# Performance work log

Hardware: AMD Instinct MI355X
Metric: run time of the kernel (lower is better)

## Reference

```python
import jax, jax.numpy as jnp
import numpy as np

NEG_INF = -1e30

def _rotary_tables(n_pos, d_k):
    # angular_freq = (1/10000)**linspace(0,1,d_k//4), padded with d_k//4 zeros -> d_k//2 freqs
    freqs = (1.0 / 10000.0) ** jnp.linspace(0.0, 1.0, d_k // 4, dtype=jnp.float32)
    freqs = jnp.concatenate([freqs, jnp.zeros(d_k // 4, dtype=jnp.float32)])  # [d_k//2]
    t = jnp.arange(n_pos, dtype=jnp.float32)
    theta = t[:, None] * freqs[None, :]  # [n_pos, d_k//2]
    return jnp.cos(theta), jnp.sin(theta)

def _apply_rotary(x_bhtd, cos, sin):
    # Faithful to torch source: cos/sin are indexed/broadcast along dim -3,
    # which for [B,H,T,D] input is the HEAD axis (original code's quirk).
    c = cos[None, :, None, :]  # [1,H,1,D/2]
    s = sin[None, :, None, :]
    x1, x2 = jnp.split(x_bhtd, 2, axis=-1)
    y1 = x1 * c + x2 * s
    y2 = -x1 * s + x2 * c
    return jnp.concatenate([y1, y2], axis=-1)

def setup_inputs() -> dict:
    key = jax.random.key(0)
    k1, k2, k3 = jax.random.split(key, 3)
    B, S, D = 4, 2048, 2048
    x = jax.random.normal(k1, (B, S, D), dtype=jnp.float32)
    Wqkv = jax.random.normal(k2, (D, 3 * D), dtype=jnp.float32) * (D ** -0.5)
    Wo = jax.random.normal(k3, (D, D), dtype=jnp.float32) * (D ** -0.5)
    return {"x": x, "Wqkv": Wqkv, "Wo": Wo, "n_heads": 16}

def reference(x, Wqkv, Wo, n_heads):
    B, S, D = x.shape
    H = int(n_heads)
    d_k = D // H
    qkv = (x @ Wqkv).reshape(B, S, 3, H, d_k)
    qkv = jnp.transpose(qkv, (2, 0, 3, 1, 4))  # [3,B,H,S,dk]
    Q, K, V = qkv[0], qkv[1], qkv[2]
    cos, sin = _rotary_tables(H, d_k)  # indexed by head axis, per original code
    Q = _apply_rotary(Q, cos, sin)
    K = _apply_rotary(K, cos, sin)
    scores = jnp.einsum('bhqd,bhkd->bhqk', Q, K) / jnp.sqrt(jnp.float32(d_k))
    causal = jnp.tril(jnp.ones((S, S), dtype=bool))
    scores = jnp.where(causal[None, None, :, :], scores, NEG_INF)
    attn = jax.nn.softmax(scores, axis=-1)
    out = jnp.einsum('bhqk,bhkd->bhqd', attn, V)  # [B,H,S,dk]
    out = jnp.transpose(out, (0, 2, 1, 3)).reshape(B, S, D)
    return out @ Wo
```

## Files before the change

kernel.cpp:

```cpp
#include <hip/hip_runtime.h>

typedef __attribute__((ext_vector_type(8))) short short8;
typedef __attribute__((ext_vector_type(4))) short short4v;
typedef __attribute__((ext_vector_type(4))) float f32x4;

__device__ inline short f2bf(float f) {
    union { float f; unsigned u; } v; v.f = f;
    unsigned r = v.u + 0x7fffu + ((v.u >> 16) & 1u);
    return (short)(r >> 16);
}

__device__ __forceinline__ void gload16(const short* g, short* l) {
    __builtin_amdgcn_global_load_lds(
        (const __attribute__((address_space(1))) unsigned int*)g,
        (__attribute__((address_space(3))) unsigned int*)l, 16, 0, 0);
}

__global__ __launch_bounds__(256) void cvt_f32_to_bf16(const float* __restrict__ in,
                                                       short* __restrict__ out, int n4) {
    int i = blockIdx.x * 256 + threadIdx.x;
    if (i >= n4) return;
    float4 v = ((const float4*)in)[i];
    short4v o;
    o[0] = f2bf(v.x); o[1] = f2bf(v.y); o[2] = f2bf(v.z); o[3] = f2bf(v.w);
    ((short4v*)out)[i] = o;
}

__global__ __launch_bounds__(256) void transpose_to_bf16(const float* __restrict__ in,
                                                         short* __restrict__ out,
                                                         int R, int C) {
    __shared__ short tile[64][66];
    int r0 = blockIdx.x * 64, c0 = blockIdx.y * 64;
    int tid = threadIdx.x;
#pragma unroll
    for (int i = 0; i < 16; i++) {
        int idx = i * 256 + tid;
        int r = idx >> 6, c = idx & 63;
        tile[r][c] = f2bf(in[(size_t)(r0 + r) * C + (c0 + c)]);
    }
    __syncthreads();
#pragma unroll
    for (int i = 0; i < 16; i++) {
        int idx = i * 256 + tid;
        int c = idx >> 6, r = idx & 63;
        out[(size_t)(c0 + c) * R + (r0 + r)] = tile[r][c];
    }
}

template <int EPI>
__global__ __launch_bounds__(512) void gemm256(const short* __restrict__ A,
                                               const short* __restrict__ Bt,
                                               int M, int N, int K,
                                               short* __restrict__ O0, short* __restrict__ O1,
                                               short* __restrict__ O2, float* __restrict__ OF,
                                               float qscale) {
    __shared__ short As[2][2][256 * 32];
    __shared__ short Bs[2][2][256 * 32];
    int tid = threadIdx.x, lane = tid & 63, wid = tid >> 6;
    int wr = wid >> 2, wc = wid & 3;
    int mtn = M >> 8;
    int band = mtn >> 3;
    int bid = blockIdx.x;
    int xcd = bid & 7, kk = bid >> 3;
    int nt = kk / band, gmr = kk % band;
    int mt = xcd * band + gmr;
    int row0 = mt << 8, col0 = nt << 8;
    int t15 = lane & 15, t4 = lane >> 4;
    int NT = K >> 6;

    f32x4 acc[8][4];
#pragma unroll
    for (int m = 0; m < 8; m++)
#pragma unroll
        for (int n = 0; n < 4; n++) acc[m][n] = (f32x4){0.f, 0.f, 0.f, 0.f};

    int sg = (lane & 3) ^ ((lane >> 3) & 3);
    int srw = lane >> 2;
    int ce = t4 ^ ((t15 >> 1) & 3);

    auto stageA = [&](int t, int kh) {
        if (t >= NT) return;
        int kb = (t << 6) + (kh << 5);
        short* dst = &As[t & 1][kh][0];
#pragma unroll
        for (int i = 0; i < 2; i++) {
            int seg = wid * 2 + i;
            int row = seg * 16 + srw;
            gload16(A + (size_t)(row0 + row) * K + kb + sg * 8, dst + seg * 512);
        }
    };
    auto stageB = [&](int t, int kh) {
        if (t >= NT) return;
        int kb = (t << 6) + (kh << 5);
        short* dst = &Bs[t & 1][kh][0];
#pragma unroll
        for (int i = 0; i < 2; i++) {
            int seg = wid * 2 + i;
            int row = seg * 16 + srw;
            gload16(Bt + (size_t)(col0 + row) * K + kb + sg * 8, dst + seg * 512);
        }
    };

    auto lda = [&](int d, int kh, short8 (&af)[8]) {
#pragma unroll
        for (int m = 0; m < 8; m++) {
            int row = wr * 128 + m * 16 + t15;
            af[m] = *(short8*)(&As[d][kh][row * 32 + ce * 8]);
        }
    };
    auto ldb = [&](int d, int kh, short8 (&bf)[4]) {
#pragma unroll
        for (int n = 0; n < 4; n++) {
            int row = wc * 64 + n * 16 + t15;
            bf[n] = *(short8*)(&Bs[d][kh][row * 32 + ce * 8]);
        }
    };

#define MFMA32(AF, BF)                                                               \
    __builtin_amdgcn_s_setprio(1);                                                   \
    _Pragma("unroll")                                                                \
    for (int m_ = 0; m_ < 8; m_++)                                                   \
        _Pragma("unroll")                                                            \
        for (int n_ = 0; n_ < 4; n_++)                                               \
            acc[m_][n_] = __builtin_amdgcn_mfma_f32_16x16x32_bf16(                   \
                AF[m_], BF[n_], acc[m_][n_], 0, 0, 0);                               \
    __builtin_amdgcn_s_setprio(0);

    stageA(0, 0); stageB(0, 0);
    stageA(0, 1); stageB(0, 1);
    asm volatile("s_waitcnt vmcnt(0)" ::: "memory");
    asm volatile("s_barrier" ::: "memory");

    for (int t = 0; t < NT; t++) {
        int d = t & 1;
        short8 af0[8], bf0[4], af1[8], bf1[4];
        lda(d, 0, af0); ldb(d, 0, bf0);
        stageA(t + 1, 0); stageB(t + 1, 0);
        stageA(t + 1, 1); stageB(t + 1, 1);
        MFMA32(af0, bf0);
        lda(d, 1, af1); ldb(d, 1, bf1);
        MFMA32(af1, bf1);
        asm volatile("s_waitcnt vmcnt(0)" ::: "memory");
        asm volatile("s_barrier" ::: "memory");
    }

#undef MFMA32

#pragma unroll
    for (int m = 0; m < 8; m++) {
#pragma unroll
        for (int n = 0; n < 4; n++) {
#pragma unroll
            for (int r = 0; r < 4; r++) {
                float v = acc[m][n][r];
                int gm2 = row0 + wr * 128 + m * 16 + t4 * 4 + r;
                int gn = col0 + wc * 64 + n * 16 + t15;
                if (EPI == 0) {
                    int part = gn >> 11, within = gn & 2047;
                    int h = within >> 7, dk = within & 127;
                    int bb = gm2 >> 11, s = gm2 & 2047;
                    int z = bb * 16 + h;
                    if (part == 0) O0[((size_t)z * 2048 + s) * 128 + dk] = f2bf(v * qscale);
                    else if (part == 1) O1[((size_t)z * 2048 + s) * 128 + dk] = f2bf(v);
                    else O2[((size_t)z * 128 + dk) * 2048 + s] = f2bf(v);
                } else {
                    OF[(size_t)gm2 * N + gn] = v;
                }
            }
        }
    }
}

__global__ __launch_bounds__(512, 4) void attn_fwd(const short* __restrict__ Q,
                                                   const short* __restrict__ Kb,
                                                   const short* __restrict__ Vt,
                                                   short* __restrict__ O) {
    __shared__ short Kls[2][64 * 128];
    __shared__ short Vls[128 * 64];
    __shared__ __align__(16) short Pls[8][16 * 64];
    int tid = threadIdx.x, lane = tid & 63, wid = tid >> 6;
    int bx = blockIdx.x, z = blockIdx.y;
    int pr = bx >> 1, hh = bx & 1;
    int qpan = (wid < 4) ? pr : (15 - pr);
    int t15 = lane & 15, t4 = lane >> 4;
    const short* Qh = Q + (size_t)z * 2048 * 128;
    const short* Kh = Kb + (size_t)z * 2048 * 128;
    const short* Vh = Vt + (size_t)z * 128 * 2048;
    int q0w = qpan * 128 + hh * 64 + (wid & 3) * 16;

    short8 qf[4];
    {
        const short* qrow = Qh + (size_t)(q0w + t15) * 128;
#pragma unroll
        for (int s = 0; s < 4; s++) qf[s] = *(const short8*)(qrow + s * 32 + t4 * 8);
    }

    f32x4 o[8];
#pragma unroll
    for (int st = 0; st < 8; st++) o[st] = (f32x4){0.f, 0.f, 0.f, 0.f};
    float m_s = -1e30f, l_s = 0.f;

    auto stageK = [&](int t, int buf) {
#pragma unroll
        for (int i = 0; i < 2; i++) {
            int seg = wid * 2 + i;
            int row = seg * 4 + t4;
            int kl = (lane & 15) ^ (row & 7);
            gload16(Kh + (size_t)(t * 64 + row) * 128 + kl * 8, &Kls[buf][seg * 512]);
        }
    };
    auto stageV = [&](int t) {
#pragma unroll
        for (int i = 0; i < 2; i++) {
            int seg = wid * 2 + i;
            int row = seg * 8 + (lane >> 3);
            int kl = (lane & 7) ^ (row & 7);
            gload16(Vh + (size_t)row * 2048 + t * 64 + kl * 8, &Vls[seg * 512]);
        }
    };

    int nt = 2 * (15 - pr) + 2;
    stageK(0, 0);
    __syncthreads();

    for (int t = 0; t < nt; t++) {
        int buf = t & 1;
        stageV(t);
        if (t + 1 < nt) stageK(t + 1, buf ^ 1);
        bool active = (t * 64 <= q0w + 15);

        if (active) {
            f32x4 sc[4];
#pragma unroll
            for (int c = 0; c < 4; c++) {
                sc[c] = (f32x4){0.f, 0.f, 0.f, 0.f};
#pragma unroll
                for (int s = 0; s < 4; s++) {
                    int row = c * 16 + t15;
                    int ck = (s * 4 + t4) ^ (row & 7);
                    short8 kf = *(short8*)(&Kls[buf][row * 128 + ck * 8]);
                    sc[c] = __builtin_amdgcn_mfma_f32_16x16x32_bf16(kf, qf[s], sc[c], 0, 0, 0);
                }
            }

            if (t * 64 + 63 > q0w) {
                int qq = q0w + t15;
#pragma unroll
                for (int c = 0; c < 4; c++)
#pragma unroll
                    for (int r = 0; r < 4; r++) {
                        int kv = t * 64 + c * 16 + t4 * 4 + r;
                        if (kv > qq) sc[c][r] = -1e30f;
                    }
            }

            float tm = fmaxf(fmaxf(fmaxf(sc[0][0], sc[0][1]), fmaxf(sc[0][2], sc[0][3])),
                             fmaxf(fmaxf(sc[1][0], sc[1][1]), fmaxf(sc[1][2], sc[1][3])));
            tm = fmaxf(tm, fmaxf(fmaxf(fmaxf(sc[2][0], sc[2][1]), fmaxf(sc[2][2], sc[2][3])),
                                 fmaxf(fmaxf(sc[3][0], sc[3][1]), fmaxf(sc[3][2], sc[3][3]))));
            bool need = (tm > m_s + 8.f);
            if (__any(need)) {
                tm = fmaxf(tm, __shfl_xor(tm, 16));
                tm = fmaxf(tm, __shfl_xor(tm, 32));
                float mn = fmaxf(m_s, tm);
                float scf = exp2f(m_s - mn);
                m_s = mn;
                l_s *= scf;
                float sr0 = __shfl(scf, t4 * 4 + 0);
                float sr1 = __shfl(scf, t4 * 4 + 1);
                float sr2 = __shfl(scf, t4 * 4 + 2);
                float sr3 = __shfl(scf, t4 * 4 + 3);
#pragma unroll
                for (int st = 0; st < 8; st++) {
                    o[st][0] *= sr0; o[st][1] *= sr1;
                    o[st][2] *= sr2; o[st][3] *= sr3;
                }
            }
            int t15l = t15 & 7;
#pragma unroll
            for (int c = 0; c < 4; c++) {
                float p0 = exp2f(sc[c][0] - m_s);
                float p1 = exp2f(sc[c][1] - m_s);
                float p2 = exp2f(sc[c][2] - m_s);
                float p3 = exp2f(sc[c][3] - m_s);
                l_s += (p0 + p1) + (p2 + p3);
                unsigned u0, u1;
                asm("v_cvt_pk_bf16_f32 %0, %1, %2" : "=v"(u0) : "v"(p0), "v"(p1));
                asm("v_cvt_pk_bf16_f32 %0, %1, %2" : "=v"(u1) : "v"(p2), "v"(p3));
                int ch = (c * 2 + (t4 >> 1)) ^ t15l;
                uint2 uu; uu.x = u0; uu.y = u1;
                *(uint2*)((char*)&Pls[wid][0] + t15 * 128 + ch * 16 + (t4 & 1) * 8) = uu;
            }
        }

        __syncthreads();

        if (active) {
            short8 pa[2];
#pragma unroll
            for (int s2 = 0; s2 < 2; s2++) {
                int ch2 = (s2 * 4 + t4) ^ (t15 & 7);
                pa[s2] = *(short8*)((char*)&Pls[wid][0] + t15 * 128 + ch2 * 16);
            }
#pragma unroll
            for (int st = 0; st < 8; st++) {
#pragma unroll
                for (int s2 = 0; s2 < 2; s2++) {
                    int row = st * 16 + t15;
                    int ck = (s2 * 4 + t4) ^ (row & 7);
                    short8 vf = *(short8*)(&Vls[row * 64 + ck * 8]);
                    o[st] = __builtin_amdgcn_mfma_f32_16x16x32_bf16(pa[s2], vf, o[st], 0, 0, 0);
                }
            }
        }

        __syncthreads();
    }

    l_s += __shfl_xor(l_s, 16);
    l_s += __shfl_xor(l_s, 32);
    float lr0 = __shfl(l_s, t4 * 4 + 0);
    float lr1 = __shfl(l_s, t4 * 4 + 1);
    float lr2 = __shfl(l_s, t4 * 4 + 2);
    float lr3 = __shfl(l_s, t4 * 4 + 3);
    float lr[4] = {lr0, lr1, lr2, lr3};

    int b = z >> 4, h = z & 15;
#pragma unroll
    for (int st = 0; st < 8; st++)
#pragma unroll
        for (int r = 0; r < 4; r++) {
            int s = q0w + t4 * 4 + r;
            float val = o[st][r] / lr[r];
            O[((size_t)b * 2048 + s) * 2048 + h * 128 + st * 16 + t15] = f2bf(val);
        }
}

extern "C" void kernel_launch(void* const* d_in, const int* in_sizes, int n_in,
                              void* d_out, int out_size, void* d_ws, size_t ws_size,
                              hipStream_t stream) {
    const float* x = (const float*)d_in[0];
    const float* Wqkv = (const float*)d_in[1];
    const float* Wo = (const float*)d_in[2];

    const int B = 4, S = 2048, D = 2048, DK = 128;
    const int M = B * S;
    const int N1 = 3 * D;
    (void)in_sizes; (void)n_in; (void)out_size; (void)ws_size;

    char* ws = (char*)d_ws;
    size_t off = 0;
    short* x_bf = (short*)(ws + off);   off += (size_t)M * D * 2;
    short* wqkv_t = (short*)(ws + off); off += (size_t)N1 * D * 2;
    short* wo_t = (short*)(ws + off);   off += (size_t)D * D * 2;
    short* Qb = (short*)(ws + off);     off += (size_t)64 * S * DK * 2;
    short* Kb = (short*)(ws + off);     off += (size_t)64 * S * DK * 2;
    short* Vt = (short*)(ws + off);     off += (size_t)64 * S * DK * 2;
    short* Ob = (short*)(ws + off);     off += (size_t)M * D * 2;

    cvt_f32_to_bf16<<<(M * D / 4 + 255) / 256, 256, 0, stream>>>(x, x_bf, M * D / 4);
    transpose_to_bf16<<<dim3(D / 64, N1 / 64, 1), 256, 0, stream>>>(Wqkv, wqkv_t, D, N1);
    transpose_to_bf16<<<dim3(D / 64, D / 64, 1), 256, 0, stream>>>(Wo, wo_t, D, D);
    gemm256<0><<<(M / 256) * (N1 / 256), 512, 0, stream>>>(
        x_bf, wqkv_t, M, N1, D, Qb, Kb, Vt, nullptr, 0.12751743553366927f);
    attn_fwd<<<dim3(16, 64), 512, 0, stream>>>(Qb, Kb, Vt, Ob);
    gemm256<1><<<(M / 256) * (D / 256), 512, 0, stream>>>(
        Ob, wo_t, M, D, D, nullptr, nullptr, nullptr, (float*)d_out, 1.0f);
}
```

Baseline: 452.6 us.

## Deepen GEMM pipeline to four-stage ring with partial vmcnt waits

Restructures the GEMM main loop from a double-buffered 64-wide K step into a 4-slot ring of 32-wide K tiles, prefetching three tiles ahead. It waits with vmcnt counts instead of draining all loads, so global-to-LDS copies stay in flight across iterations and memory latency is better hidden. The cost is twice as many barriers per K and a tighter LDS-reuse ordering that depends on exact vmcnt accounting. LDS footprint stays the same.

Measured after the change: 436.2 us. -3.6%, faster.

```diff
diff --git a/kernel.cpp b/kernel.cpp
--- a/kernel.cpp
+++ b/kernel.cpp
@@ -54,8 +54,8 @@
                                                short* __restrict__ O0, short* __restrict__ O1,
                                                short* __restrict__ O2, float* __restrict__ OF,
                                                float qscale) {
-    __shared__ short As[2][2][256 * 32];
-    __shared__ short Bs[2][2][256 * 32];
+    __shared__ short As[4][256 * 32];
+    __shared__ short Bs[4][256 * 32];
     int tid = threadIdx.x, lane = tid & 63, wid = tid >> 6;
     int wr = wid >> 2, wc = wid & 3;
     int mtn = M >> 8;
@@ -66,7 +66,7 @@
     int mt = xcd * band + gmr;
     int row0 = mt << 8, col0 = nt << 8;
     int t15 = lane & 15, t4 = lane >> 4;
-    int NT = K >> 6;
+    int NT = K >> 5;
 
     f32x4 acc[8][4];
 #pragma unroll
@@ -78,10 +78,10 @@
     int srw = lane >> 2;
     int ce = t4 ^ ((t15 >> 1) & 3);
 
-    auto stageA = [&](int t, int kh) {
+    auto stageA = [&](int t) {
         if (t >= NT) return;
-        int kb = (t << 6) + (kh << 5);
-        short* dst = &As[t & 1][kh][0];
+        int kb = t << 5;
+        short* dst = &As[t & 3][0];
 #pragma unroll
         for (int i = 0; i < 2; i++) {
             int seg = wid * 2 + i;
@@ -89,10 +89,10 @@
             gload16(A + (size_t)(row0 + row) * K + kb + sg * 8, dst + seg * 512);
         }
     };
-    auto stageB = [&](int t, int kh) {
+    auto stageB = [&](int t) {
         if (t >= NT) return;
-        int kb = (t << 6) + (kh << 5);
-        short* dst = &Bs[t & 1][kh][0];
+        int kb = t << 5;
+        short* dst = &Bs[t & 3][0];
 #pragma unroll
         for (int i = 0; i < 2; i++) {
             int seg = wid * 2 + i;
@@ -101,50 +101,40 @@
         }
     };
 
-    auto lda = [&](int d, int kh, short8 (&af)[8]) {
+    stageA(0); stageB(0);
+    stageA(1); stageB(1);
+    stageA(2); stageB(2);
+    asm volatile("s_waitcnt vmcnt(8)" ::: "memory");
+    asm volatile("s_barrier" ::: "memory");
+
+    for (int t = 0; t < NT; t++) {
+        int bufi = t & 3;
+        short8 af[8], bf[4];
 #pragma unroll
         for (int m = 0; m < 8; m++) {
             int row = wr * 128 + m * 16 + t15;
-            af[m] = *(short8*)(&As[d][kh][row * 32 + ce * 8]);
-        }
-    };
-    auto ldb = [&](int d, int kh, short8 (&bf)[4]) {
+            af[m] = *(short8*)(&As[bufi][row * 32 + ce * 8]);
+        }
 #pragma unroll
         for (int n = 0; n < 4; n++) {
             int row = wc * 64 + n * 16 + t15;
-            bf[n] = *(short8*)(&Bs[d][kh][row * 32 + ce * 8]);
-        }
-    };
-
-#define MFMA32(AF, BF)                                                               \
-    __builtin_amdgcn_s_setprio(1);                                                   \
-    _Pragma("unroll")                                                                \
-    for (int m_ = 0; m_ < 8; m_++)                                                   \
-        _Pragma("unroll")                                                            \
-        for (int n_ = 0; n_ < 4; n_++)                                               \
-            acc[m_][n_] = __builtin_amdgcn_mfma_f32_16x16x32_bf16(                   \
-                AF[m_], BF[n_], acc[m_][n_], 0, 0, 0);                               \
-    __builtin_amdgcn_s_setprio(0);
-
-    stageA(0, 0); stageB(0, 0);
-    stageA(0, 1); stageB(0, 1);
-    asm volatile("s_waitcnt vmcnt(0)" ::: "memory");
-    asm volatile("s_barrier" ::: "memory");
-
-    for (int t = 0; t < NT; t++) {
-        int d = t & 1;
-        short8 af0[8], bf0[4], af1[8], bf1[4];
-        lda(d, 0, af0); ldb(d, 0, bf0);
-        stageA(t + 1, 0); stageB(t + 1, 0);
-        stageA(t + 1, 1); stageB(t + 1, 1);
-        MFMA32(af0, bf0);
-        lda(d, 1, af1); ldb(d, 1, bf1);
-        MFMA32(af1, bf1);
-        asm volatile("s_waitcnt vmcnt(0)" ::: "memory");
+            bf[n] = *(short8*)(&Bs[bufi][row * 32 + ce * 8]);
+        }
+        stageA(t + 3); stageB(t + 3);
+
+        __builtin_amdgcn_s_setprio(1);
+#pragma unroll
+        for (int m = 0; m < 8; m++)
+#pragma unroll
+            for (int n = 0; n < 4; n++)
+                acc[m][n] = __builtin_amdgcn_mfma_f32_16x16x32_bf16(af[m], bf[n], acc[m][n], 0, 0, 0);
+        __builtin_amdgcn_s_setprio(0);
+
+        if (t + 3 < NT)       asm volatile("s_waitcnt vmcnt(8)" ::: "memory");
+        else if (t + 3 == NT) asm volatile("s_waitcnt vmcnt(4)" ::: "memory");
+        else                  asm volatile("s_waitcnt vmcnt(0)" ::: "memory");
         asm volatile("s_barrier" ::: "memory");
     }
-
-#undef MFMA32
 
 #pragma unroll
     for (int m = 0; m < 8; m++) {
```
